# Kernel optimization log

Measured on AMD Instinct MI355X. Metric: run time of the kernel, lower is better.

## Reference

```python
import jax, jax.numpy as jnp
import numpy as np

E, CAP, D, H = 8, 2048, 1024, 4096  # experts, capacity, model_dim, hidden

def setup_inputs() -> dict:
    key = jax.random.key(0)
    k = jax.random.split(key, 5)
    s1 = 1.0 / np.sqrt(D)
    s2 = 1.0 / np.sqrt(H)
    return {
        "x": jax.random.normal(k[0], (E, CAP, D), dtype=jnp.float32),
        "fc1_w": jax.random.uniform(k[1], (E, H, D), jnp.float32, -s1, s1),
        "fc1_b": jax.random.uniform(k[2], (E, H), jnp.float32, -s1, s1),
        "fc2_w": jax.random.uniform(k[3], (E, H, D), jnp.float32, -s2, s2),
        "fc2_b": jax.random.uniform(k[4], (E, D), jnp.float32, -s2, s2),
    }

def reference(x, fc1_w, fc1_b, fc2_w, fc2_b):
    # y = relu(x @ fc1_w^T + b1) @ fc2_w + b2, batched over experts e
    y = jnp.einsum('ecd,ehd->ech', x, fc1_w) + fc1_b[:, None, :]   # [E, CAP, H]
    y = jax.nn.relu(y)
    y = jnp.einsum('ech,ehd->ecd', y, fc2_w) + fc2_b[:, None, :]   # [E, CAP, D]
    return y
```

## Files before the change

kernel.cpp:

```cpp
#include <hip/hip_runtime.h>
#include <hip/hip_bf16.h>
#include <stdint.h>

#define E_    8
#define CAP_  2048
#define D_    1024
#define H_    4096

typedef unsigned short u16;
typedef __attribute__((ext_vector_type(8))) short bf16x8;
typedef __attribute__((ext_vector_type(4))) float f32x4;

__device__ __forceinline__ u16 f2bf(float f) {
    union { float f; unsigned int u; } v; v.f = f;
    unsigned int u = v.u;
    unsigned int r = (u + 0x7fffu + ((u >> 16) & 1u)) >> 16;
    return (u16)r;
}

__device__ __forceinline__ void gload_lds16(const void* g, void* l) {
    __builtin_amdgcn_global_load_lds(
        (const __attribute__((address_space(1))) unsigned int*)g,
        (__attribute__((address_space(3))) unsigned int*)l,
        16, 0, 0);
}

__global__ void cvt_f32_bf16(const float* __restrict__ in, u16* __restrict__ out, int n4) {
    int i = blockIdx.x * blockDim.x + threadIdx.x;
    if (i >= n4) return;
    const float4 v = ((const float4*)in)[i];
    ushort4 o;
    o.x = f2bf(v.x); o.y = f2bf(v.y); o.z = f2bf(v.z); o.w = f2bf(v.w);
    ((ushort4*)out)[i] = o;
}

__global__ void transpose_cvt(const float* __restrict__ in, u16* __restrict__ out) {
    __shared__ float t[64][69];
    const int e  = blockIdx.z;
    const int h0 = blockIdx.y * 64;
    const int d0 = blockIdx.x * 64;
    const float* I = in + (size_t)e * H_ * D_;
    u16* O = out + (size_t)e * D_ * H_;
    const int tid = threadIdx.x;
    const int r  = tid >> 4;
    const int c  = (tid & 15) * 4;
    #pragma unroll
    for (int s = 0; s < 4; ++s) {
        const int h = r + s * 16;
        const float4 v = *(const float4*)&I[(size_t)(h0 + h) * D_ + d0 + c];
        t[h][c] = v.x; t[h][c + 1] = v.y; t[h][c + 2] = v.z; t[h][c + 3] = v.w;
    }
    __syncthreads();
    #pragma unroll
    for (int s = 0; s < 4; ++s) {
        const int d = r + s * 16;
        ushort4 o;
        o.x = f2bf(t[c + 0][d]); o.y = f2bf(t[c + 1][d]);
        o.z = f2bf(t[c + 2][d]); o.w = f2bf(t[c + 3][d]);
        *(ushort4*)&O[(size_t)(d0 + d) * H_ + h0 + c] = o;
    }
}

template<int EPI>
__global__ __launch_bounds__(512, 2) void gemm256(
    const u16* __restrict__ A, const u16* __restrict__ B,
    const float* __restrict__ bias, void* __restrict__ Cv,
    int M, int N, int K, int TM, int TN,
    size_t sA, size_t sB, size_t sBias, size_t sC)
{
    __shared__ __align__(16) u16 lds[2][2][2][128 * 64];

    const int nwg = gridDim.x;
    const int cpx = nwg >> 3;
    const int bid = blockIdx.x;
    const int wg  = (bid & 7) * cpx + (bid >> 3);
    const int tpe = TM * TN;
    const int e   = wg / tpe;
    const int rem = wg - e * tpe;
    const int tn  = rem / TM;
    const int tm  = rem - tn * TM;
    const int row0 = tm << 8;
    const int col0 = tn << 8;

    const u16* Ae = A + (size_t)e * sA;
    const u16* Be = B + (size_t)e * sB;

    const int tid  = threadIdx.x;
    const int lane = tid & 63;
    const int w    = tid >> 6;
    const int wr   = w >> 2;
    const int wc   = w & 3;
    const int wcH  = wc >> 1;
    const int wcL  = wc & 1;
    const int fr   = lane & 15;
    const int fq   = lane >> 4;
    const int cx   = (fq ^ (fr & 7)) << 4;
    const int lo0  = fr * 128 + cx;
    const int lo1  = fr * 128 + (cx ^ 64);
    const int sl   = lane ^ ((lane >> 3) & 7);
    const int NT   = K >> 6;

    const int srow = (w << 4) + (sl >> 3);
    const int scol = (sl & 7) << 3;
    const u16* pA[2][2];
    const u16* pB[2][2];
    #pragma unroll
    for (int l = 0; l < 2; ++l)
        #pragma unroll
        for (int hf = 0; hf < 2; ++hf) {
            pA[l][hf] = Ae + (size_t)(row0 + hf * 128 + srow + l * 8) * K + scol;
            pB[l][hf] = Be + (size_t)(col0 + hf * 128 + srow + l * 8) * K + scol;
        }

    auto stage = [&](int buf, bool pred) {
        #pragma unroll
        for (int l = 0; l < 2; ++l)
            #pragma unroll
            for (int hf = 0; hf < 2; ++hf) {
                if (pred) {
                    gload_lds16(pA[l][hf], &lds[buf][0][hf][(w * 2 + l) * 512]);
                    gload_lds16(pB[l][hf], &lds[buf][1][hf][(w * 2 + l) * 512]);
                }
                pA[l][hf] += 64;
                pB[l][hf] += 64;
            }
    };

    f32x4 acc[8][4] = {};

    stage(0, true);
    asm volatile("s_waitcnt vmcnt(0)");
    __builtin_amdgcn_s_barrier();

    for (int t = 0; t < NT; ++t) {
        const int db = t & 1;
        const char* Ah = (const char*)&lds[db][0][wr][0];
        const char* Bh = (const char*)&lds[db][1][wcH][0];

        auto rdA = [&](bf16x8 (&a)[2][2], int p) {
            #pragma unroll
            for (int mm = 0; mm < 2; ++mm) {
                a[mm][0] = *(const bf16x8*)(Ah + (2 * p + mm) * 2048 + lo0);
                a[mm][1] = *(const bf16x8*)(Ah + (2 * p + mm) * 2048 + lo1);
            }
        };

        bf16x8 b[4][2];
        #pragma unroll
        for (int n = 0; n < 4; ++n) {
            b[n][0] = *(const bf16x8*)(Bh + wcL * 8192 + n * 2048 + lo0);
            b[n][1] = *(const bf16x8*)(Bh + wcL * 8192 + n * 2048 + lo1);
        }

        auto domfma = [&](bf16x8 (&a)[2][2], int p) {
            __builtin_amdgcn_s_setprio(1);
            #pragma unroll
            for (int kk = 0; kk < 2; ++kk)
                #pragma unroll
                for (int mm = 0; mm < 2; ++mm)
                    #pragma unroll
                    for (int n = 0; n < 4; ++n)
                        acc[2 * p + mm][n] = __builtin_amdgcn_mfma_f32_16x16x32_bf16(
                            a[mm][kk], b[n][kk], acc[2 * p + mm][n], 0, 0, 0);
            __builtin_amdgcn_s_setprio(0);
        };

        bf16x8 aA[2][2], aB[2][2];
        rdA(aA, 0);
        stage(db ^ 1, t + 1 < NT);
        rdA(aB, 1); domfma(aA, 0);
        rdA(aA, 2); domfma(aB, 1);
        rdA(aB, 3); domfma(aA, 2);
        domfma(aB, 3);

        asm volatile("s_waitcnt vmcnt(0)");
        __builtin_amdgcn_s_barrier();
    }

    const float* be = bias + (size_t)e * sBias;
    if (EPI == 0) {
        u16* cl = (u16*)&lds[0][0][0][0];
        #pragma unroll
        for (int n = 0; n < 4; ++n) {
            const int ccol = wc * 64 + n * 16 + fr;
            const float bv = be[col0 + ccol];
            #pragma unroll
            for (int m = 0; m < 8; ++m) {
                const int crow = wr * 128 + m * 16 + fq * 4;
                #pragma unroll
                for (int i = 0; i < 4; ++i) {
                    float v = acc[m][n][i] + bv;
                    v = v > 0.f ? v : 0.f;
                    cl[(crow + i) * 256 + ccol] = f2bf(v);
                }
            }
        }
        __builtin_amdgcn_s_barrier();
        u16* Ce = (u16*)Cv + (size_t)e * sC;
        const int rr = tid >> 5;
        const int cc = (tid & 31) * 8;
        #pragma unroll
        for (int s = 0; s < 16; ++s) {
            const int row = s * 16 + rr;
            const float4 v = *(const float4*)&cl[row * 256 + cc];
            *(float4*)&Ce[(size_t)(row0 + row) * N + col0 + cc] = v;
        }
    } else {
        float* cf = (float*)&lds[0][0][0][0];
        float* Ce = (float*)Cv + (size_t)e * sC;
        #pragma unroll
        for (int p = 0; p < 2; ++p) {
            __builtin_amdgcn_s_barrier();
            #pragma unroll
            for (int n = 0; n < 4; ++n) {
                const int ccol = wc * 64 + n * 16 + fr;
                const float bv = be[col0 + ccol];
                #pragma unroll
                for (int mm = 0; mm < 4; ++mm) {
                    const int lrow = wr * 64 + mm * 16 + fq * 4;
                    #pragma unroll
                    for (int i = 0; i < 4; ++i)
                        cf[(lrow + i) * 256 + ccol] = acc[p * 4 + mm][n][i] + bv;
                }
            }
            __builtin_amdgcn_s_barrier();
            const int lr = tid >> 6;
            const int cc = (tid & 63) * 4;
            #pragma unroll
            for (int s = 0; s < 16; ++s) {
                const int lrow = s * 8 + lr;
                const int wrr  = lrow >> 6;
                const int rem2 = lrow & 63;
                const int grow = row0 + wrr * 128 + p * 64 + rem2;
                const float4 v = *(const float4*)&cf[lrow * 256 + cc];
                *(float4*)&Ce[(size_t)grow * N + col0 + cc] = v;
            }
        }
    }
}

extern "C" void kernel_launch(void* const* d_in, const int* in_sizes, int n_in,
                              void* d_out, int out_size, void* d_ws, size_t ws_size,
                              hipStream_t stream) {
    (void)in_sizes; (void)n_in; (void)out_size; (void)ws_size;
    const float* x     = (const float*)d_in[0];
    const float* fc1_w = (const float*)d_in[1];
    const float* fc1_b = (const float*)d_in[2];
    const float* fc2_w = (const float*)d_in[3];
    const float* fc2_b = (const float*)d_in[4];
    float* out = (float*)d_out;

    u16* xbf  = (u16*)d_ws;
    u16* w1bf = xbf  + (size_t)E_ * CAP_ * D_;
    u16* w2t  = w1bf + (size_t)E_ * H_ * D_;
    u16* y1   = w2t  + (size_t)E_ * D_ * H_;

    {
        int n4 = E_ * CAP_ * D_ / 4;
        cvt_f32_bf16<<<n4 / 256, 256, 0, stream>>>(x, xbf, n4);
    }
    {
        int n4 = E_ * H_ * D_ / 4;
        cvt_f32_bf16<<<n4 / 256, 256, 0, stream>>>(fc1_w, w1bf, n4);
    }
    transpose_cvt<<<dim3(D_ / 64, H_ / 64, E_), 256, 0, stream>>>(fc2_w, w2t);

    gemm256<0><<<dim3(E_ * (CAP_ / 256) * (H_ / 256)), 512, 0, stream>>>(
        xbf, w1bf, fc1_b, y1, CAP_, H_, D_, CAP_ / 256, H_ / 256,
        (size_t)CAP_ * D_, (size_t)H_ * D_, (size_t)H_, (size_t)CAP_ * H_);

    gemm256<1><<<dim3(E_ * (CAP_ / 256) * (D_ / 256)), 512, 0, stream>>>(
        y1, w2t, fc2_b, out, CAP_, D_, H_, CAP_ / 256, D_ / 256,
        (size_t)CAP_ * H_, (size_t)D_ * H_, (size_t)D_, (size_t)CAP_ * D_);
}
```

Before: 366.4 us.

## Shrink GEMM tile to 256x128 with K=32 stages for higher occupancy

Replaces the 256x256 tile with 64-wide K steps by a 256x128 tile with 32-wide K steps. LDS use falls to 64 KB, and launch bounds now target 4 blocks per CU instead of 2. The tile index order changes to row-major, and the LDS swizzle and epilogue are rewritten for the smaller tile. Each tile now does half the MFMA work per byte loaded, which lowers data reuse and doubles the barriers per unit of K work. The intent is to gain occupancy and latency hiding in exchange. The software interleaving of LDS reads with MFMAs inside each K step is dropped in favour of a simple load-then-compute loop.

```diff
diff --git a/kernel.cpp b/kernel.cpp
--- a/kernel.cpp
+++ b/kernel.cpp
@@ -62,13 +62,13 @@
 }
 
 template<int EPI>
-__global__ __launch_bounds__(512, 2) void gemm256(
+__global__ __launch_bounds__(512, 4) void gemm128(
     const u16* __restrict__ A, const u16* __restrict__ B,
     const float* __restrict__ bias, void* __restrict__ Cv,
     int M, int N, int K, int TM, int TN,
     size_t sA, size_t sB, size_t sBias, size_t sC)
 {
-    __shared__ __align__(16) u16 lds[2][2][2][128 * 64];
+    __shared__ __align__(16) u16 lds[32768];
 
     const int nwg = gridDim.x;
     const int cpx = nwg >> 3;
@@ -77,10 +77,10 @@
     const int tpe = TM * TN;
     const int e   = wg / tpe;
     const int rem = wg - e * tpe;
-    const int tn  = rem / TM;
-    const int tm  = rem - tn * TM;
+    const int tm  = rem / TN;
+    const int tn  = rem - tm * TN;
     const int row0 = tm << 8;
-    const int col0 = tn << 8;
+    const int col0 = tn << 7;
 
     const u16* Ae = A + (size_t)e * sA;
     const u16* Be = B + (size_t)e * sB;
@@ -88,45 +88,30 @@
     const int tid  = threadIdx.x;
     const int lane = tid & 63;
     const int w    = tid >> 6;
-    const int wr   = w >> 2;
-    const int wc   = w & 3;
-    const int wcH  = wc >> 1;
-    const int wcL  = wc & 1;
+    const int wr   = w >> 1;
+    const int wc   = w & 1;
     const int fr   = lane & 15;
     const int fq   = lane >> 4;
-    const int cx   = (fq ^ (fr & 7)) << 4;
-    const int lo0  = fr * 128 + cx;
-    const int lo1  = fr * 128 + (cx ^ 64);
-    const int sl   = lane ^ ((lane >> 3) & 7);
-    const int NT   = K >> 6;
-
-    const int srow = (w << 4) + (sl >> 3);
-    const int scol = (sl & 7) << 3;
-    const u16* pA[2][2];
-    const u16* pB[2][2];
-    #pragma unroll
-    for (int l = 0; l < 2; ++l)
-        #pragma unroll
-        for (int hf = 0; hf < 2; ++hf) {
-            pA[l][hf] = Ae + (size_t)(row0 + hf * 128 + srow + l * 8) * K + scol;
-            pB[l][hf] = Be + (size_t)(col0 + hf * 128 + srow + l * 8) * K + scol;
-        }
+    const int L    = fr * 64 + ((fq ^ ((fr >> 1) & 3)) << 4);
+    const int NT   = K >> 5;
+
+    const int arow = tid >> 2;
+    const int kel  = (((tid & 3) ^ ((tid >> 3) & 3)) << 3);
+    const u16* pA0 = Ae + (size_t)(row0 + arow) * K + kel;
+    const u16* pA1 = Ae + (size_t)(row0 + 128 + arow) * K + kel;
+    const u16* pB0 = Be + (size_t)(col0 + arow) * K + kel;
 
     auto stage = [&](int buf, bool pred) {
-        #pragma unroll
-        for (int l = 0; l < 2; ++l)
-            #pragma unroll
-            for (int hf = 0; hf < 2; ++hf) {
-                if (pred) {
-                    gload_lds16(pA[l][hf], &lds[buf][0][hf][(w * 2 + l) * 512]);
-                    gload_lds16(pB[l][hf], &lds[buf][1][hf][(w * 2 + l) * 512]);
-                }
-                pA[l][hf] += 64;
-                pB[l][hf] += 64;
-            }
+        u16* base = lds + buf * 12288;
+        if (pred) {
+            gload_lds16(pA0, base + tid * 8);
+            gload_lds16(pA1, base + 4096 + tid * 8);
+            gload_lds16(pB0, base + 8192 + tid * 8);
+        }
+        pA0 += 32; pA1 += 32; pB0 += 32;
     };
 
-    f32x4 acc[8][4] = {};
+    f32x4 acc[4][4] = {};
 
     stage(0, true);
     asm volatile("s_waitcnt vmcnt(0)");
@@ -134,44 +119,27 @@
 
     for (int t = 0; t < NT; ++t) {
         const int db = t & 1;
-        const char* Ah = (const char*)&lds[db][0][wr][0];
-        const char* Bh = (const char*)&lds[db][1][wcH][0];
-
-        auto rdA = [&](bf16x8 (&a)[2][2], int p) {
+        const char* Ab = (const char*)lds + db * 24576;
+        const char* Bb = Ab + 16384;
+
+        stage(db ^ 1, t + 1 < NT);
+
+        bf16x8 b[4], a[4];
+        #pragma unroll
+        for (int n = 0; n < 4; ++n)
+            b[n] = *(const bf16x8*)(Bb + wc * 4096 + n * 1024 + L);
+        #pragma unroll
+        for (int m = 0; m < 4; ++m)
+            a[m] = *(const bf16x8*)(Ab + wr * 4096 + m * 1024 + L);
+
+        __builtin_amdgcn_s_setprio(1);
+        #pragma unroll
+        for (int m = 0; m < 4; ++m)
             #pragma unroll
-            for (int mm = 0; mm < 2; ++mm) {
-                a[mm][0] = *(const bf16x8*)(Ah + (2 * p + mm) * 2048 + lo0);
-                a[mm][1] = *(const bf16x8*)(Ah + (2 * p + mm) * 2048 + lo1);
-            }
-        };
-
-        bf16x8 b[4][2];
-        #pragma unroll
-        for (int n = 0; n < 4; ++n) {
-            b[n][0] = *(const bf16x8*)(Bh + wcL * 8192 + n * 2048 + lo0);
-            b[n][1] = *(const bf16x8*)(Bh + wcL * 8192 + n * 2048 + lo1);
-        }
-
-        auto domfma = [&](bf16x8 (&a)[2][2], int p) {
-            __builtin_amdgcn_s_setprio(1);
-            #pragma unroll
-            for (int kk = 0; kk < 2; ++kk)
-                #pragma unroll
-                for (int mm = 0; mm < 2; ++mm)
-                    #pragma unroll
-                    for (int n = 0; n < 4; ++n)
-                        acc[2 * p + mm][n] = __builtin_amdgcn_mfma_f32_16x16x32_bf16(
-                            a[mm][kk], b[n][kk], acc[2 * p + mm][n], 0, 0, 0);
-            __builtin_amdgcn_s_setprio(0);
-        };
-
-        bf16x8 aA[2][2], aB[2][2];
-        rdA(aA, 0);
-        stage(db ^ 1, t + 1 < NT);
-        rdA(aB, 1); domfma(aA, 0);
-        rdA(aA, 2); domfma(aB, 1);
-        rdA(aB, 3); domfma(aA, 2);
-        domfma(aB, 3);
+            for (int n = 0; n < 4; ++n)
+                acc[m][n] = __builtin_amdgcn_mfma_f32_16x16x32_bf16(
+                    a[m], b[n], acc[m][n], 0, 0, 0);
+        __builtin_amdgcn_s_setprio(0);
 
         asm volatile("s_waitcnt vmcnt(0)");
         __builtin_amdgcn_s_barrier();
@@ -179,60 +147,60 @@
 
     const float* be = bias + (size_t)e * sBias;
     if (EPI == 0) {
-        u16* cl = (u16*)&lds[0][0][0][0];
+        u16* cl = lds;
         #pragma unroll
         for (int n = 0; n < 4; ++n) {
             const int ccol = wc * 64 + n * 16 + fr;
             const float bv = be[col0 + ccol];
             #pragma unroll
-            for (int m = 0; m < 8; ++m) {
-                const int crow = wr * 128 + m * 16 + fq * 4;
+            for (int m = 0; m < 4; ++m) {
+                const int crow = wr * 64 + m * 16 + fq * 4;
                 #pragma unroll
                 for (int i = 0; i < 4; ++i) {
                     float v = acc[m][n][i] + bv;
                     v = v > 0.f ? v : 0.f;
-                    cl[(crow + i) * 256 + ccol] = f2bf(v);
+                    cl[(crow + i) * 128 + ccol] = f2bf(v);
                 }
             }
         }
         __builtin_amdgcn_s_barrier();
         u16* Ce = (u16*)Cv + (size_t)e * sC;
-        const int rr = tid >> 5;
-        const int cc = (tid & 31) * 8;
-        #pragma unroll
-        for (int s = 0; s < 16; ++s) {
-            const int row = s * 16 + rr;
-            const float4 v = *(const float4*)&cl[row * 256 + cc];
+        const int rr = tid >> 4;
+        const int cc = (tid & 15) * 8;
+        #pragma unroll
+        for (int s = 0; s < 8; ++s) {
+            const int row = s * 32 + rr;
+            const float4 v = *(const float4*)&cl[row * 128 + cc];
             *(float4*)&Ce[(size_t)(row0 + row) * N + col0 + cc] = v;
         }
     } else {
-        float* cf = (float*)&lds[0][0][0][0];
+        float* cf = (float*)lds;
         float* Ce = (float*)Cv + (size_t)e * sC;
         #pragma unroll
         for (int p = 0; p < 2; ++p) {
             __builtin_amdgcn_s_barrier();
-            #pragma unroll
-            for (int n = 0; n < 4; ++n) {
-                const int ccol = wc * 64 + n * 16 + fr;
-                const float bv = be[col0 + ccol];
+            if ((wr >> 1) == p) {
                 #pragma unroll
-                for (int mm = 0; mm < 4; ++mm) {
-                    const int lrow = wr * 64 + mm * 16 + fq * 4;
+                for (int n = 0; n < 4; ++n) {
+                    const int ccol = wc * 64 + n * 16 + fr;
+                    const float bv = be[col0 + ccol];
                     #pragma unroll
-                    for (int i = 0; i < 4; ++i)
-                        cf[(lrow + i) * 256 + ccol] = acc[p * 4 + mm][n][i] + bv;
+                    for (int m = 0; m < 4; ++m) {
+                        const int lrow = (wr & 1) * 64 + m * 16 + fq * 4;
+                        #pragma unroll
+                        for (int i = 0; i < 4; ++i)
+                            cf[(lrow + i) * 128 + ccol] = acc[m][n][i] + bv;
+                    }
                 }
             }
             __builtin_amdgcn_s_barrier();
-            const int lr = tid >> 6;
-            const int cc = (tid & 63) * 4;
+            const int lr = tid >> 5;
+            const int cc = (tid & 31) * 4;
             #pragma unroll
-            for (int s = 0; s < 16; ++s) {
-                const int lrow = s * 8 + lr;
-                const int wrr  = lrow >> 6;
-                const int rem2 = lrow & 63;
-                const int grow = row0 + wrr * 128 + p * 64 + rem2;
-                const float4 v = *(const float4*)&cf[lrow * 256 + cc];
+            for (int s = 0; s < 8; ++s) {
+                const int lrow = s * 16 + lr;
+                const int grow = row0 + p * 128 + lrow;
+                const float4 v = *(const float4*)&cf[lrow * 128 + cc];
                 *(float4*)&Ce[(size_t)grow * N + col0 + cc] = v;
             }
         }
@@ -265,11 +233,11 @@
     }
     transpose_cvt<<<dim3(D_ / 64, H_ / 64, E_), 256, 0, stream>>>(fc2_w, w2t);
 
-    gemm256<0><<<dim3(E_ * (CAP_ / 256) * (H_ / 256)), 512, 0, stream>>>(
-        xbf, w1bf, fc1_b, y1, CAP_, H_, D_, CAP_ / 256, H_ / 256,
+    gemm128<0><<<dim3(E_ * (CAP_ / 256) * (H_ / 128)), 512, 0, stream>>>(
+        xbf, w1bf, fc1_b, y1, CAP_, H_, D_, CAP_ / 256, H_ / 128,
         (size_t)CAP_ * D_, (size_t)H_ * D_, (size_t)H_, (size_t)CAP_ * H_);
 
-    gemm256<1><<<dim3(E_ * (CAP_ / 256) * (D_ / 256)), 512, 0, stream>>>(
-        y1, w2t, fc2_b, out, CAP_, D_, H_, CAP_ / 256, D_ / 256,
+    gemm128<1><<<dim3(E_ * (CAP_ / 256) * (D_ / 128)), 512, 0, stream>>>(
+        y1, w2t, fc2_b, out, CAP_, D_, H_, CAP_ / 256, D_ / 128,
         (size_t)CAP_ * H_, (size_t)D_ * H_, (size_t)D_, (size_t)CAP_ * D_);
 }
```

Measured after the change: 393.8 us. 1.07x slower.
